# Kernel tuning notes

Measured on AMD Instinct MI355X. Metric: run time of the kernel, lower is better.

Reference implementation:

```python
import jax, jax.numpy as jnp
import numpy as np

NEG_INF = -(2.0**32) + 1.0  # matches tf: -2**32 + 1


def _positional_encoding(seq_len, d_model):
    # sinusoidal PE exactly as in the module (sin on even cols, cos on odd cols)
    pos = np.arange(seq_len)[:, None].astype(np.float32)
    i = np.arange(d_model)[None, :]
    angle_rates = 1.0 / np.power(10000.0, 2 * (i // 2) / np.float32(d_model))
    ang = pos * angle_rates
    ang[:, 0::2] = np.sin(ang[:, 0::2])
    ang[:, 1::2] = np.cos(ang[:, 1::2])
    return jnp.asarray(ang[None, ...], dtype=jnp.float32)  # [1, S, D]


def setup_inputs() -> dict:
    key = jax.random.key(0)
    kq, kk, kv, kw, km = jax.random.split(key, 5)
    B, S, D = 64, 512, 256
    q = jax.random.normal(kq, (B, S, D), dtype=jnp.float32)
    k = jax.random.normal(kk, (B, S, D), dtype=jnp.float32)
    v = jax.random.normal(kv, (B, S, D), dtype=jnp.float32)
    # keras 'random_uniform' initializer default range is [-0.05, 0.05]
    W = jax.random.uniform(kw, (D, D), dtype=jnp.float32, minval=-0.05, maxval=0.05)
    mask = jax.random.randint(km, (B, S), 0, 2, dtype=jnp.int32)
    return {"q": q, "k": k, "v": v, "W": W, "mask": mask}


def reference(q, k, v, W, mask):
    B, S, D = q.shape
    pe = _positional_encoding(S, D)  # [1, S, D]
    q = q + pe
    k = k + pe
    q = jax.nn.relu(jnp.einsum('bsd,de->bse', q, W))
    k = jax.nn.relu(jnp.einsum('bsd,de->bse', k, W))
    logits = jnp.einsum('bqd,bkd->bqk', q, k) / jnp.sqrt(jnp.float32(D))  # [B,S,S]
    # mask over key positions, broadcast across query dim
    logits = jnp.where(mask[:, None, :] == 0, jnp.float32(NEG_INF), logits)
    att = jax.nn.softmax(logits, axis=-1)
    out = jnp.einsum('bqk,bkd->bqd', att, v)
    return jnp.mean(out, axis=1)  # [B, D]
```

## Files before the change

### kernel.cpp

```cpp
#include <hip/hip_runtime.h>

#define NEG_INF (-4294967295.0f)

typedef _Float16 f16;
typedef _Float16 f16x8 __attribute__((ext_vector_type(8)));
typedef _Float16 f16x4v __attribute__((ext_vector_type(4)));
typedef float f32x4 __attribute__((ext_vector_type(4)));

#define MFMA16(a,b,c) __builtin_amdgcn_mfma_f32_16x16x32_f16((a),(b),(c),0,0,0)

#if defined(__has_builtin)
#if __has_builtin(__builtin_amdgcn_global_load_lds)
#define HAS_GLD 1
#endif
#endif

__device__ __forceinline__ void stage16(const void* g, void* lds_base, int lane) {
#ifdef HAS_GLD
    __builtin_amdgcn_global_load_lds(
        (const __attribute__((address_space(1))) unsigned int*)g,
        (__attribute__((address_space(3))) unsigned int*)lds_base, 16, 0, 0);
#else
    ((f16x8*)lds_base)[lane] = *(const f16x8*)g;
#endif
}

__global__ __launch_bounds__(256) void pe_kernel(float* __restrict__ pe) {
    int idx = blockIdx.x * 256 + threadIdx.x;
    int s = idx >> 8, d = idx & 255;
    float x = (float)(d & ~1) * (1.f / 256.f);
    float rate = exp2f(x * -13.287712379549449f);
    float ang = (float)s * rate;
    pe[idx] = (d & 1) ? cosf(ang) : sinf(ang);
}

__global__ __launch_bounds__(256) void wt_kernel(const float* __restrict__ W,
                                                 f16* __restrict__ WT) {
    int e = blockIdx.x, d = threadIdx.x;
    WT[(e << 8) + d] = (f16)W[(d << 8) + e];
}

__global__ __launch_bounds__(256) void vt_kernel(const float* __restrict__ V,
                                                 f16* __restrict__ VT) {
    __shared__ float T[64 * 269];
    const int t = threadIdx.x;
    const int k0 = blockIdx.x * 64, bb = blockIdx.y;
    #pragma unroll
    for (int it = 0; it < 16; ++it) {
        int r = it * 4 + (t >> 6), d = (t & 63) * 4;
        float4 v = *(const float4*)(V + (((size_t)(bb * 512 + k0 + r)) << 8) + d);
        T[r * 269 + d + 0] = v.x; T[r * 269 + d + 1] = v.y;
        T[r * 269 + d + 2] = v.z; T[r * 269 + d + 3] = v.w;
    }
    __syncthreads();
    #pragma unroll
    for (int dr = 0; dr < 8; ++dr) {
        int d = dr * 32 + (t >> 3), c = t & 7;
        f16x8 o;
        #pragma unroll
        for (int j = 0; j < 8; ++j) o[j] = (f16)T[(c * 8 + j) * 269 + d];
        *(f16x8*)(VT + (((size_t)(bb * 256 + d)) << 9) + k0 + c * 8) = o;
    }
}

__global__ __launch_bounds__(256) void proj_kernel(const float* __restrict__ q,
                                                   const float* __restrict__ k,
                                                   const f16* __restrict__ WT,
                                                   const float* __restrict__ pe,
                                                   f16* __restrict__ outp) {
    __shared__ __align__(16) f16 As[2][64 * 64];
    __shared__ __align__(16) f16 WTs[2][256 * 64];
    const int t = threadIdx.x, l = t & 63, wv = t >> 6, lr = l & 15, lg = l >> 4;
    const int r0 = blockIdx.x * 64;
    const float* src = (r0 < 32768) ? q : k;
    const int rb = r0 & 32767;

    float4 av[4], pv[4];
    auto loadA = [&](int kc) {
        #pragma unroll
        for (int it = 0; it < 4; ++it) {
            int r = it * 16 + (t >> 4), d = (t & 15) * 4;
            av[it] = *(const float4*)(src + (size_t)(rb + r) * 256 + kc * 64 + d);
            pv[it] = *(const float4*)(pe + ((rb + r) & 511) * 256 + kc * 64 + d);
        }
    };
    auto writeA = [&](int dst) {
        #pragma unroll
        for (int it = 0; it < 4; ++it) {
            int r = it * 16 + (t >> 4), d = (t & 15) * 4;
            f16x4v h;
            h[0] = (f16)(av[it].x + pv[it].x); h[1] = (f16)(av[it].y + pv[it].y);
            h[2] = (f16)(av[it].z + pv[it].z); h[3] = (f16)(av[it].w + pv[it].w);
            *(f16x4v*)&As[dst][(r << 6) + (d ^ ((r & 7) << 3))] = h;
        }
    };
    auto stageW = [&](int dst, int kc) {
        #pragma unroll
        for (int it = 0; it < 8; ++it) {
            int eb = wv * 64 + it * 8;
            int e = eb + (l >> 3), c = l & 7;
            const f16* s = WT + (e << 8) + kc * 64 + ((c ^ (e & 7)) << 3);
            stage16(s, &WTs[dst][eb << 6], l);
        }
    };

    f32x4 acc[16] = {};
    loadA(0); stageW(0, 0); writeA(0);
    __syncthreads();

    for (int kc = 0; kc < 4; ++kc) {
        int cur = kc & 1;
        if (kc < 3) { loadA(kc + 1); stageW(cur ^ 1, kc + 1); }
        #pragma unroll
        for (int kk = 0; kk < 2; ++kk) {
            int dk = kk * 32 + lg * 8;
            f16x8 a = *(const f16x8*)&As[cur][((wv * 16 + lr) << 6) + (dk ^ ((lr & 7) << 3))];
            #pragma unroll
            for (int nt = 0; nt < 16; ++nt) {
                int e = nt * 16 + lr;
                f16x8 b = *(const f16x8*)&WTs[cur][(e << 6) + (dk ^ ((lr & 7) << 3))];
                acc[nt] = MFMA16(a, b, acc[nt]);
            }
        }
        if (kc < 3) { writeA(cur ^ 1); __syncthreads(); }
    }

    f16* Rb = &WTs[0][0] + wv * 4096;
    #pragma unroll
    for (int nt = 0; nt < 16; ++nt) {
        #pragma unroll
        for (int rg = 0; rg < 4; ++rg) {
            int rr = lg * 4 + rg, col = nt * 16 + lr;
            float v = acc[nt][rg];
            v = v > 0.f ? v * 0.25f : 0.f;
            Rb[rr * 256 + ((((col >> 3) ^ (rr & 7)) << 3) | (col & 7))] = (f16)v;
        }
    }
    #pragma unroll
    for (int it = 0; it < 8; ++it) {
        int row = it * 2 + (l >> 5), c = l & 31;
        f16x8 v8 = *(const f16x8*)&Rb[row * 256 + ((c ^ (row & 7)) << 3)];
        *(f16x8*)(outp + (((size_t)(r0 + wv * 16 + row)) << 8) + c * 8) = v8;
    }
}

__global__ __launch_bounds__(256) void attn_kernel(const f16* __restrict__ QP,
                                                   const f16* __restrict__ KP,
                                                   const f16* __restrict__ VT,
                                                   const int* __restrict__ mask,
                                                   float* __restrict__ out) {
    __shared__ __align__(16) f16 Ks[2][32 * 256];
    __shared__ __align__(16) f16 Vs[2][256 * 32];
    __shared__ __align__(16) f16 Pw[4][16 * 32];
    const int t = threadIdx.x, l = t & 63, wv = t >> 6, lr = l & 15, lg = l >> 4;
    const int n = blockIdx.x, bb = n & 63, qt = n >> 6;
    const int q0 = qt * 64 + wv * 16;
    const int* maskb = mask + bb * 512;

    auto stageK = [&](int dst, int kt) {
        #pragma unroll
        for (int it = 0; it < 4; ++it) {
            int r2 = wv * 8 + it * 2;
            int r = r2 + (l >> 5), c = l & 31;
            const f16* s = KP + (((size_t)(bb * 512 + kt * 32 + r)) << 8) + ((c ^ (r & 7)) << 3);
            stage16(s, &Ks[dst][r2 << 8], l);
        }
    };
    auto stageV = [&](int dst, int kt) {
        #pragma unroll
        for (int it = 0; it < 4; ++it) {
            int db = wv * 64 + it * 16;
            int d = db + (l >> 2), c = l & 3;
            const f16* s = VT + (((size_t)(bb * 256 + d)) << 9) + kt * 32 + (c << 3);
            stage16(s, &Vs[dst][db << 5], l);
        }
    };

    f16x8 qf[8];
    const f16* qrow = QP + (((size_t)(bb * 512 + q0 + lr)) << 8);
    #pragma unroll
    for (int kk = 0; kk < 8; ++kk) qf[kk] = *(const f16x8*)(qrow + kk * 32 + lg * 8);

    f32x4 O[16] = {};
    float m[4], ls[4];
    #pragma unroll
    for (int r = 0; r < 4; ++r) { m[r] = -INFINITY; ls[r] = 0.f; }

    int mk0c = maskb[lr], mk1c = maskb[16 + lr], mk0n = 0, mk1n = 0;
    stageK(0, 0); stageV(0, 0);
    __syncthreads();

    for (int kt = 0; kt < 16; ++kt) {
        const int cur = kt & 1;
        if (kt < 15) {
            stageK(cur ^ 1, kt + 1);
            stageV(cur ^ 1, kt + 1);
            mk0n = maskb[(kt + 1) * 32 + lr];
            mk1n = maskb[(kt + 1) * 32 + 16 + lr];
        }
        f32x4 s0 = {}, s1 = {};
        #pragma unroll
        for (int kk = 0; kk < 8; ++kk) {
            int dk = kk * 32 + lg * 8;
            f16x8 b0 = *(const f16x8*)&Ks[cur][(lr << 8) + (dk ^ ((lr & 7) << 3))];
            f16x8 b1 = *(const f16x8*)&Ks[cur][((16 + lr) << 8) + (dk ^ ((lr & 7) << 3))];
            s0 = MFMA16(qf[kk], b0, s0);
            s1 = MFMA16(qf[kk], b1, s1);
        }
        float fsc[4];
        #pragma unroll
        for (int rg = 0; rg < 4; ++rg) {
            float v0 = mk0c ? s0[rg] : NEG_INF;
            float v1 = mk1c ? s1[rg] : NEG_INF;
            float tm = fmaxf(v0, v1);
            tm = fmaxf(tm, __shfl_xor(tm, 1));
            tm = fmaxf(tm, __shfl_xor(tm, 2));
            tm = fmaxf(tm, __shfl_xor(tm, 4));
            tm = fmaxf(tm, __shfl_xor(tm, 8));
            float mn = fmaxf(m[rg], tm);
            float f = __expf(m[rg] - mn);
            float p0 = __expf(v0 - mn);
            float p1 = __expf(v1 - mn);
            float rs = p0 + p1;
            rs += __shfl_xor(rs, 1);
            rs += __shfl_xor(rs, 2);
            rs += __shfl_xor(rs, 4);
            rs += __shfl_xor(rs, 8);
            ls[rg] = ls[rg] * f + rs;
            m[rg] = mn; fsc[rg] = f;
            int qq = lg * 4 + rg;
            Pw[wv][(qq << 5) + (lr ^ ((qq & 3) << 3))] = (f16)p0;
            Pw[wv][(qq << 5) + ((16 + lr) ^ ((qq & 3) << 3))] = (f16)p1;
        }
        #pragma unroll
        for (int nt = 0; nt < 16; ++nt) {
            #pragma unroll
            for (int rg = 0; rg < 4; ++rg) O[nt][rg] *= fsc[rg];
        }
        f16x8 pa = *(const f16x8*)&Pw[wv][(lr << 5) + ((lg * 8) ^ ((lr & 3) << 3))];
        #pragma unroll
        for (int nt = 0; nt < 16; ++nt) {
            f16x8 vb = *(const f16x8*)&Vs[cur][((nt * 16 + lr) << 5) + lg * 8];
            O[nt] = MFMA16(pa, vb, O[nt]);
        }
        if (kt < 15) { __syncthreads(); mk0c = mk0n; mk1c = mk1n; }
    }

    float rls[4];
    #pragma unroll
    for (int rg = 0; rg < 4; ++rg) rls[rg] = 1.0f / ls[rg];
    #pragma unroll
    for (int nt = 0; nt < 16; ++nt) {
        float v = 0.f;
        #pragma unroll
        for (int rg = 0; rg < 4; ++rg) v += O[nt][rg] * rls[rg];
        v += __shfl_xor(v, 16);
        v += __shfl_xor(v, 32);
        if (l < 16) atomicAdd(&out[bb * 256 + nt * 16 + l], v * (1.f / 512.f));
    }
}

extern "C" void kernel_launch(void* const* d_in, const int* in_sizes, int n_in,
                              void* d_out, int out_size, void* d_ws, size_t ws_size,
                              hipStream_t stream) {
    const float* q  = (const float*)d_in[0];
    const float* k  = (const float*)d_in[1];
    const float* v  = (const float*)d_in[2];
    const float* W  = (const float*)d_in[3];
    const int* mask = (const int*)d_in[4];

    f16*   QP = (f16*)d_ws;
    f16*   KP = QP + (size_t)32768 * 256;
    f16*   VT = KP + (size_t)32768 * 256;
    float* PE = (float*)((char*)d_ws + (size_t)48 * 1024 * 1024);
    f16*   WT = (f16*)((char*)d_ws + (size_t)48 * 1024 * 1024 + 512 * 1024);

    pe_kernel<<<512, 256, 0, stream>>>(PE);
    wt_kernel<<<256, 256, 0, stream>>>(W, WT);
    vt_kernel<<<dim3(8, 64), 256, 0, stream>>>(v, VT);
    proj_kernel<<<1024, 256, 0, stream>>>(q, k, WT, PE, QP);
    hipMemsetAsync(d_out, 0, 64 * 256 * sizeof(float), stream);
    attn_kernel<<<512, 256, 0, stream>>>(QP, KP, VT, mask, (float*)d_out);
}
```

Baseline: 201.7 us.

## Sum attention weights over queries, then apply one weighted reduction over V

```diff
diff --git a/kernel.cpp b/kernel.cpp
--- a/kernel.cpp
+++ b/kernel.cpp
@@ -38,29 +38,6 @@
                                                  f16* __restrict__ WT) {
     int e = blockIdx.x, d = threadIdx.x;
     WT[(e << 8) + d] = (f16)W[(d << 8) + e];
-}
-
-__global__ __launch_bounds__(256) void vt_kernel(const float* __restrict__ V,
-                                                 f16* __restrict__ VT) {
-    __shared__ float T[64 * 269];
-    const int t = threadIdx.x;
-    const int k0 = blockIdx.x * 64, bb = blockIdx.y;
-    #pragma unroll
-    for (int it = 0; it < 16; ++it) {
-        int r = it * 4 + (t >> 6), d = (t & 63) * 4;
-        float4 v = *(const float4*)(V + (((size_t)(bb * 512 + k0 + r)) << 8) + d);
-        T[r * 269 + d + 0] = v.x; T[r * 269 + d + 1] = v.y;
-        T[r * 269 + d + 2] = v.z; T[r * 269 + d + 3] = v.w;
-    }
-    __syncthreads();
-    #pragma unroll
-    for (int dr = 0; dr < 8; ++dr) {
-        int d = dr * 32 + (t >> 3), c = t & 7;
-        f16x8 o;
-        #pragma unroll
-        for (int j = 0; j < 8; ++j) o[j] = (f16)T[(c * 8 + j) * 269 + d];
-        *(f16x8*)(VT + (((size_t)(bb * 256 + d)) << 9) + k0 + c * 8) = o;
-    }
 }
 
 __global__ __launch_bounds__(256) void proj_kernel(const float* __restrict__ q,
@@ -146,12 +123,10 @@
 
 __global__ __launch_bounds__(256) void attn_kernel(const f16* __restrict__ QP,
                                                    const f16* __restrict__ KP,
-                                                   const f16* __restrict__ VT,
                                                    const int* __restrict__ mask,
-                                                   float* __restrict__ out) {
+                                                   float* __restrict__ wglob) {
     __shared__ __align__(16) f16 Ks[2][32 * 256];
-    __shared__ __align__(16) f16 Vs[2][256 * 32];
-    __shared__ __align__(16) f16 Pw[4][16 * 32];
+    __shared__ float ws[4][512];
     const int t = threadIdx.x, l = t & 63, wv = t >> 6, lr = l & 15, lg = l >> 4;
     const int n = blockIdx.x, bb = n & 63, qt = n >> 6;
     const int q0 = qt * 64 + wv * 16;
@@ -166,38 +141,29 @@
             stage16(s, &Ks[dst][r2 << 8], l);
         }
     };
-    auto stageV = [&](int dst, int kt) {
-        #pragma unroll
-        for (int it = 0; it < 4; ++it) {
-            int db = wv * 64 + it * 16;
-            int d = db + (l >> 2), c = l & 3;
-            const f16* s = VT + (((size_t)(bb * 256 + d)) << 9) + kt * 32 + (c << 3);
-            stage16(s, &Vs[dst][db << 5], l);
-        }
-    };
 
     f16x8 qf[8];
     const f16* qrow = QP + (((size_t)(bb * 512 + q0 + lr)) << 8);
     #pragma unroll
     for (int kk = 0; kk < 8; ++kk) qf[kk] = *(const f16x8*)(qrow + kk * 32 + lg * 8);
 
-    f32x4 O[16] = {};
-    float m[4], ls[4];
-    #pragma unroll
-    for (int r = 0; r < 4; ++r) { m[r] = -INFINITY; ls[r] = 0.f; }
-
-    int mk0c = maskb[lr], mk1c = maskb[16 + lr], mk0n = 0, mk1n = 0;
-    stageK(0, 0); stageV(0, 0);
+    unsigned mb0 = 0, mb1 = 0;
+    #pragma unroll
+    for (int kt = 0; kt < 16; ++kt) {
+        mb0 |= (maskb[kt * 32 + lr] ? 1u : 0u) << kt;
+        mb1 |= (maskb[kt * 32 + 16 + lr] ? 1u : 0u) << kt;
+    }
+
+    float lacc[4] = {0.f, 0.f, 0.f, 0.f};
+    f16 Pst[16][8];
+
+    stageK(0, 0);
     __syncthreads();
 
+    #pragma unroll
     for (int kt = 0; kt < 16; ++kt) {
         const int cur = kt & 1;
-        if (kt < 15) {
-            stageK(cur ^ 1, kt + 1);
-            stageV(cur ^ 1, kt + 1);
-            mk0n = maskb[(kt + 1) * 32 + lr];
-            mk1n = maskb[(kt + 1) * 32 + 16 + lr];
-        }
+        if (kt < 15) stageK(cur ^ 1, kt + 1);
         f32x4 s0 = {}, s1 = {};
         #pragma unroll
         for (int kk = 0; kk < 8; ++kk) {
@@ -207,57 +173,66 @@
             s0 = MFMA16(qf[kk], b0, s0);
             s1 = MFMA16(qf[kk], b1, s1);
         }
-        float fsc[4];
         #pragma unroll
         for (int rg = 0; rg < 4; ++rg) {
-            float v0 = mk0c ? s0[rg] : NEG_INF;
-            float v1 = mk1c ? s1[rg] : NEG_INF;
-            float tm = fmaxf(v0, v1);
-            tm = fmaxf(tm, __shfl_xor(tm, 1));
-            tm = fmaxf(tm, __shfl_xor(tm, 2));
-            tm = fmaxf(tm, __shfl_xor(tm, 4));
-            tm = fmaxf(tm, __shfl_xor(tm, 8));
-            float mn = fmaxf(m[rg], tm);
-            float f = __expf(m[rg] - mn);
-            float p0 = __expf(v0 - mn);
-            float p1 = __expf(v1 - mn);
-            float rs = p0 + p1;
-            rs += __shfl_xor(rs, 1);
-            rs += __shfl_xor(rs, 2);
-            rs += __shfl_xor(rs, 4);
-            rs += __shfl_xor(rs, 8);
-            ls[rg] = ls[rg] * f + rs;
-            m[rg] = mn; fsc[rg] = f;
-            int qq = lg * 4 + rg;
-            Pw[wv][(qq << 5) + (lr ^ ((qq & 3) << 3))] = (f16)p0;
-            Pw[wv][(qq << 5) + ((16 + lr) ^ ((qq & 3) << 3))] = (f16)p1;
-        }
-        #pragma unroll
-        for (int nt = 0; nt < 16; ++nt) {
-            #pragma unroll
-            for (int rg = 0; rg < 4; ++rg) O[nt][rg] *= fsc[rg];
-        }
-        f16x8 pa = *(const f16x8*)&Pw[wv][(lr << 5) + ((lg * 8) ^ ((lr & 3) << 3))];
-        #pragma unroll
-        for (int nt = 0; nt < 16; ++nt) {
-            f16x8 vb = *(const f16x8*)&Vs[cur][((nt * 16 + lr) << 5) + lg * 8];
-            O[nt] = MFMA16(pa, vb, O[nt]);
-        }
-        if (kt < 15) { __syncthreads(); mk0c = mk0n; mk1c = mk1n; }
-    }
-
-    float rls[4];
-    #pragma unroll
-    for (int rg = 0; rg < 4; ++rg) rls[rg] = 1.0f / ls[rg];
-    #pragma unroll
-    for (int nt = 0; nt < 16; ++nt) {
-        float v = 0.f;
-        #pragma unroll
-        for (int rg = 0; rg < 4; ++rg) v += O[nt][rg] * rls[rg];
-        v += __shfl_xor(v, 16);
-        v += __shfl_xor(v, 32);
-        if (l < 16) atomicAdd(&out[bb * 256 + nt * 16 + l], v * (1.f / 512.f));
-    }
+            float p0 = __expf(((mb0 >> kt) & 1) ? s0[rg] : NEG_INF);
+            float p1 = __expf(((mb1 >> kt) & 1) ? s1[rg] : NEG_INF);
+            f16 h0 = (f16)p0, h1 = (f16)p1;
+            Pst[kt][rg] = h0;
+            Pst[kt][4 + rg] = h1;
+            lacc[rg] += (float)h0 + (float)h1;
+        }
+        if (kt < 15) __syncthreads();
+    }
+
+    #pragma unroll
+    for (int rg = 0; rg < 4; ++rg) {
+        float s = lacc[rg];
+        s += __shfl_xor(s, 1); s += __shfl_xor(s, 2);
+        s += __shfl_xor(s, 4); s += __shfl_xor(s, 8);
+        lacc[rg] = s;
+    }
+    float rl[4];
+    float bsum = 0.f;
+    #pragma unroll
+    for (int rg = 0; rg < 4; ++rg) {
+        if (lacc[rg] > 0.f) { rl[rg] = 1.0f / lacc[rg]; }
+        else                { rl[rg] = 0.f; bsum += 1.f / 512.f; }
+    }
+
+    #pragma unroll
+    for (int kt = 0; kt < 16; ++kt) {
+        float w0 = (float)Pst[kt][0] * rl[0] + (float)Pst[kt][1] * rl[1]
+                 + (float)Pst[kt][2] * rl[2] + (float)Pst[kt][3] * rl[3] + bsum;
+        float w1 = (float)Pst[kt][4] * rl[0] + (float)Pst[kt][5] * rl[1]
+                 + (float)Pst[kt][6] * rl[2] + (float)Pst[kt][7] * rl[3] + bsum;
+        w0 += __shfl_xor(w0, 16); w0 += __shfl_xor(w0, 32);
+        w1 += __shfl_xor(w1, 16); w1 += __shfl_xor(w1, 32);
+        if (lg == 0) {
+            ws[wv][kt * 32 + lr] = w0;
+            ws[wv][kt * 32 + 16 + lr] = w1;
+        }
+    }
+    __syncthreads();
+    #pragma unroll
+    for (int i = 0; i < 2; ++i) {
+        int kk = t + i * 256;
+        float s = ws[0][kk] + ws[1][kk] + ws[2][kk] + ws[3][kk];
+        atomicAdd(&wglob[bb * 512 + kk], s);
+    }
+}
+
+__global__ __launch_bounds__(256) void wv_kernel(const float* __restrict__ wglob,
+                                                 const float* __restrict__ V,
+                                                 float* __restrict__ out) {
+    const int n = blockIdx.x, bb = n & 63, ks = n >> 6;
+    const int d = threadIdx.x;
+    const float* wr = wglob + bb * 512 + ks * 64;
+    const float* vb = V + ((((size_t)bb) * 512 + ks * 64) << 8) + d;
+    float acc = 0.f;
+    #pragma unroll 8
+    for (int kk = 0; kk < 64; ++kk) acc = fmaf(wr[kk], vb[(size_t)kk << 8], acc);
+    atomicAdd(&out[bb * 256 + d], acc * (1.f / 512.f));
 }
 
 extern "C" void kernel_launch(void* const* d_in, const int* in_sizes, int n_in,
@@ -269,16 +244,18 @@
     const float* W  = (const float*)d_in[3];
     const int* mask = (const int*)d_in[4];
 
-    f16*   QP = (f16*)d_ws;
-    f16*   KP = QP + (size_t)32768 * 256;
-    f16*   VT = KP + (size_t)32768 * 256;
-    float* PE = (float*)((char*)d_ws + (size_t)48 * 1024 * 1024);
-    f16*   WT = (f16*)((char*)d_ws + (size_t)48 * 1024 * 1024 + 512 * 1024);
+    char* ws = (char*)d_ws;
+    f16*   QP = (f16*)ws;
+    f16*   KP = (f16*)(ws + 16777216);
+    float* PE = (float*)(ws + 33554432);
+    f16*   WT = (f16*)(ws + 34078720);
+    float* WG = (float*)(ws + 34209792);
 
     pe_kernel<<<512, 256, 0, stream>>>(PE);
     wt_kernel<<<256, 256, 0, stream>>>(W, WT);
-    vt_kernel<<<dim3(8, 64), 256, 0, stream>>>(v, VT);
     proj_kernel<<<1024, 256, 0, stream>>>(q, k, WT, PE, QP);
-    hipMemsetAsync(d_out, 0, 64 * 256 * sizeof(float), stream);
-    attn_kernel<<<512, 256, 0, stream>>>(QP, KP, VT, mask, (float*)d_out);
-}
+    (void)hipMemsetAsync(WG, 0, 64 * 512 * sizeof(float), stream);
+    (void)hipMemsetAsync(d_out, 0, 64 * 256 * sizeof(float), stream);
+    attn_kernel<<<512, 256, 0, stream>>>(QP, KP, mask, WG);
+    wv_kernel<<<512, 256, 0, stream>>>(WG, v, (float*)d_out);
+}
```

After: 179.8 us. 1.12x faster.
